# Kernel optimization log

Measured on AMD Instinct MI355X. Metric: run time of the kernel, lower is better.

## Reference

```python
import jax, jax.numpy as jnp
import numpy as np

GRID_SIZE = 3
SPLINE_ORDER = 3

def make_grid():
    # grid_range=[-1,1], h=2/grid_size; extended grid of length grid_size+2k+1 = 10
    h = 2.0 / GRID_SIZE
    return (jnp.arange(-SPLINE_ORDER, GRID_SIZE + SPLINE_ORDER + 1, dtype=jnp.float32) * h - 1.0)

def b_splines(x, grid):
    # x: [N, F] -> bases [N, F, grid_size+spline_order]
    xg = x[..., None]
    bases = ((xg >= grid[:-1]) & (xg < grid[1:])).astype(x.dtype)
    for j in range(1, SPLINE_ORDER + 1):
        left = (xg - grid[: -(j + 1)]) / (grid[j:-1] - grid[: -(j + 1)])
        right = (grid[j + 1:] - xg) / (grid[j + 1:] - grid[1:-j])
        bases = left * bases[..., :-1] + right * bases[..., 1:]
    return bases

def kan_linear(x, base_w, spline_w, scaler, grid):
    # x: [N, F]; base_w: [O, F]; spline_w: [O, F, G]; scaler: [O, F]
    base = jax.nn.silu(x) @ base_w.T
    sb = b_splines(x, grid)                      # [N, F, G]
    spl = jnp.einsum('nfg,ofg->no', sb, spline_w * scaler[..., None])
    return base + spl

def kan_conv3x3(x, base_w, spline_w, scaler, grid):
    # x: [B, C, H, W]; 3x3 kernel, pad 1, stride 1 -> [B, O, H, W]
    B, C, H, W = x.shape
    patches = jax.lax.conv_general_dilated_patches(
        x, (3, 3), (1, 1), ((1, 1), (1, 1)))     # [B, C*9, H, W]
    p = patches.transpose(0, 2, 3, 1).reshape(B * H * W, C * 9)
    y = kan_linear(p, base_w, spline_w, scaler, grid)
    return y.reshape(B, H, W, -1).transpose(0, 3, 1, 2)

def maxpool2(x):
    return jax.lax.reduce_window(x, -jnp.inf, jax.lax.max,
                                 (1, 1, 2, 2), (1, 1, 2, 2), 'VALID')

def setup_inputs() -> dict:
    key = jax.random.key(0)
    ks = jax.random.split(key, 12)
    s = 0.1
    return {
        'x': jax.random.normal(ks[0], (256, 3, 32, 32), jnp.float32),
        'c1_base_w': jax.random.normal(ks[1], (8, 27), jnp.float32) * s,
        'c1_spline_w': jax.random.normal(ks[2], (8, 27, 6), jnp.float32) * s,
        'c1_scaler': jax.random.normal(ks[3], (8, 27), jnp.float32) * s,
        'c2_base_w': jax.random.normal(ks[4], (16, 72), jnp.float32) * s,
        'c2_spline_w': jax.random.normal(ks[5], (16, 72, 6), jnp.float32) * s,
        'c2_scaler': jax.random.normal(ks[6], (16, 72), jnp.float32) * s,
        'c3_base_w': jax.random.normal(ks[7], (32, 144), jnp.float32) * s,
        'c3_spline_w': jax.random.normal(ks[8], (32, 144, 6), jnp.float32) * s,
        'c3_scaler': jax.random.normal(ks[9], (32, 144), jnp.float32) * s,
        'lin_w': jax.random.normal(ks[10], (100, 512), jnp.float32) * s,
        'lin_b': jax.random.normal(ks[11], (100,), jnp.float32) * s,
    }

def reference(x, c1_base_w, c1_spline_w, c1_scaler,
              c2_base_w, c2_spline_w, c2_scaler,
              c3_base_w, c3_spline_w, c3_scaler,
              lin_w, lin_b):
    grid = make_grid()
    h = maxpool2(kan_conv3x3(x, c1_base_w, c1_spline_w, c1_scaler, grid))   # [B,8,16,16]
    h = maxpool2(kan_conv3x3(h, c2_base_w, c2_spline_w, c2_scaler, grid))   # [B,16,8,8]
    h = maxpool2(kan_conv3x3(h, c3_base_w, c3_spline_w, c3_scaler, grid))   # [B,32,4,4]
    h = h.reshape(h.shape[0], -1)                                           # [B,512]
    return h @ lin_w.T + lin_b                                              # [B,100]
```

## Files before the change

### kernel.cpp

```cpp
#include <hip/hip_runtime.h>
#include <math.h>


#define BATCH 256

typedef short bf16x8 __attribute__((ext_vector_type(8)));
typedef float f32x4  __attribute__((ext_vector_type(4)));

__device__ __forceinline__ unsigned f2bf(float f) {
    unsigned u = __float_as_uint(f);
    u += 0x7fffu + ((u >> 16) & 1u);
    return u >> 16;
}
__device__ __forceinline__ unsigned pk2(float a, float b) {
    return f2bf(a) | (f2bf(b) << 16);
}

__device__ __forceinline__ void bspline_basis(float x, float bs[6]) {
    const float h = 2.0f / 3.0f;
    float g[10];
#pragma unroll
    for (int i = 0; i < 10; ++i) g[i] = (float)(i - 3) * h - 1.0f;
    float b[9];
#pragma unroll
    for (int i = 0; i < 9; ++i) b[i] = (x >= g[i] && x < g[i + 1]) ? 1.0f : 0.0f;
#pragma unroll
    for (int j = 1; j <= 3; ++j) {
        const float inv_d = 1.0f / ((float)j * h);
#pragma unroll
        for (int i = 0; i + j < 9; ++i) {
            float left  = (x - g[i]) * inv_d;
            float right = (g[i + j + 1] - x) * inv_d;
            b[i] = left * b[i] + right * b[i + 1];
        }
    }
#pragma unroll
    for (int i = 0; i < 6; ++i) bs[i] = b[i];
}

__device__ __forceinline__ uint4 act_record(float val) {
    float silu = val / (1.0f + __expf(-val));
    float bs[6];
    bspline_basis(val, bs);
    uint4 r;
    r.x = pk2(silu, bs[0]);
    r.y = pk2(bs[1], bs[2]);
    r.z = pk2(bs[3], bs[4]);
    r.w = f2bf(bs[5]);
    return r;
}

__device__ __forceinline__ uint4 fuse_w(const float* bw, const float* sw,
                                        const float* sc, int j) {
    float s = sc[j];
    uint4 r;
    r.x = pk2(bw[j],             sw[j * 6 + 0] * s);
    r.y = pk2(sw[j * 6 + 1] * s, sw[j * 6 + 2] * s);
    r.z = pk2(sw[j * 6 + 3] * s, sw[j * 6 + 4] * s);
    r.w = f2bf(sw[j * 6 + 5] * s);
    return r;
}

__global__ __launch_bounds__(512, 4) void kan_l1(
        const float* __restrict__ x,
        const float* __restrict__ bw, const float* __restrict__ sw,
        const float* __restrict__ sc,
        const float* __restrict__ bw3, const float* __restrict__ sw3,
        const float* __restrict__ sc3,
        uint4* __restrict__ w3g,
        float* __restrict__ out) {
    constexpr int C = 3, H = 32, W = 32, F = 27, FP = 28, NS = 7;
    constexpr int RT = 18, TC = 34, NT = 512;

    __shared__ uint4 s_act[C * RT * TC];
    __shared__ uint4 s_w[FP * 16];

    const int tid = threadIdx.x;
    const int bid = blockIdx.x;
    const int b   = bid >> 1;
    const int v   = bid & 1;

    if (bid < 9) {
        int i = bid * NT + tid;
        if (i < 4608) {
            int o = i / 144, fp = i % 144;
            w3g[fp * 32 + o] = fuse_w(bw3, sw3, sc3, i);
        }
    }

    for (int i = tid; i < FP * 16; i += NT) {
        int fp = i >> 4, o = i & 15;
        uint4 r = make_uint4(0u, 0u, 0u, 0u);
        if (fp < F && o < 8) r = fuse_w(bw, sw, sc, o * F + fp);
        s_w[i] = r;
    }

    const int r0 = 16 * v - 1;
    const float* xb = x + (size_t)b * C * H * W;
    for (int i = tid; i < C * RT * TC; i += NT) {
        int cc  = i / (RT * TC);
        int rr  = (i / TC) % RT;
        int col = i % TC;
        int gr = r0 + rr, gc = col - 1;
        float val = 0.0f;
        if ((unsigned)gr < (unsigned)H && (unsigned)gc < (unsigned)W)
            val = xb[(cc * H + gr) * W + gc];
        s_act[i] = act_record(val);
    }
    __syncthreads();

    const int lane = tid & 63;
    const int wv   = tid >> 6;
    const int kg   = lane >> 4;
    const int oc   = lane & 15;
    const int m    = lane & 15;

    bf16x8 bfr[NS];
#pragma unroll
    for (int s = 0; s < NS; ++s)
        bfr[s] = *reinterpret_cast<const bf16x8*>(&s_w[(4 * s + kg) * 16 + oc]);

    int pixoff[4];
#pragma unroll
    for (int t = 0; t < 4; ++t)
        pixoff[t] = (2 * wv + (t >> 1)) * TC + 16 * (t & 1) + m;

    f32x4 acc[4];
#pragma unroll
    for (int t = 0; t < 4; ++t) acc[t] = (f32x4){0.f, 0.f, 0.f, 0.f};

#pragma unroll
    for (int s = 0; s < NS; ++s) {
        int tp = 4 * s + kg;
        tp = (tp > F - 1) ? F - 1 : tp;
        int c  = tp / 9;
        int t9 = tp - 9 * c;
        int ky = t9 / 3;
        int kx = t9 - 3 * ky;
        int base = (c * RT + ky) * TC + kx;
#pragma unroll
        for (int t = 0; t < 4; ++t) {
            bf16x8 a = *reinterpret_cast<const bf16x8*>(&s_act[base + pixoff[t]]);
            acc[t] = __builtin_amdgcn_mfma_f32_16x16x32_bf16(a, bfr[s], acc[t], 0, 0, 0);
        }
    }

    if (oc < 8) {
        f32x4 e0, e1;
#pragma unroll
        for (int p = 0; p < 4; ++p) {
            e0[p] = fmaxf(acc[0][p], acc[2][p]);
            e1[p] = fmaxf(acc[1][p], acc[3][p]);
        }
        float* op = out + (((size_t)b * 8 + oc) * 16 + (8 * v + wv)) * 16;
        op[2 * kg]         = fmaxf(e0[0], e0[1]);
        op[2 * kg + 1]     = fmaxf(e0[2], e0[3]);
        op[8 + 2 * kg]     = fmaxf(e1[0], e1[1]);
        op[8 + 2 * kg + 1] = fmaxf(e1[2], e1[3]);
    }
}

__global__ __launch_bounds__(512, 2) void kan_l2l3lin(
        const float* __restrict__ h1,
        const float* __restrict__ bw2, const float* __restrict__ sw2,
        const float* __restrict__ sc2,
        const uint4* __restrict__ w3g,
        const float* __restrict__ lin_w, const float* __restrict__ lin_b,
        float* __restrict__ out) {
    constexpr int NT = 512;
    __shared__ alignas(16) unsigned char s_mem[59904];
    uint4* s_act2 = (uint4*)s_mem;
    uint4* s_w2   = (uint4*)(s_mem + 41472);
    float* s_h2   = (float*)s_mem;
    uint4* s_act3 = (uint4*)(s_mem + 4096);
    float* s_h3   = (float*)s_mem;

    const int tid = threadIdx.x;
    const int n   = blockIdx.x;
    const int lane = tid & 63;
    const int wv   = tid >> 6;
    const int kg   = lane >> 4;
    const int oc   = lane & 15;
    const int m    = lane & 15;

    for (int i = tid; i < 72 * 16; i += NT) {
        int fp = i >> 4, o = i & 15;
        s_w2[i] = fuse_w(bw2, sw2, sc2, o * 72 + fp);
    }
    const float* xb = h1 + (size_t)n * 8 * 16 * 16;
    for (int i = tid; i < 8 * 18 * 18; i += NT) {
        int cc  = i / 324;
        int rr  = (i / 18) % 18;
        int col = i % 18;
        int gr = rr - 1, gc = col - 1;
        float val = 0.0f;
        if ((unsigned)gr < 16u && (unsigned)gc < 16u)
            val = xb[(cc * 16 + gr) * 16 + gc];
        s_act2[i] = act_record(val);
    }
    __syncthreads();

    {
        bf16x8 bfr2[18];
#pragma unroll
        for (int s = 0; s < 18; ++s)
            bfr2[s] = *reinterpret_cast<const bf16x8*>(&s_w2[(4 * s + kg) * 16 + oc]);
        const int p0 = (2 * wv) * 18 + m;
        const int p1 = p0 + 18;
        f32x4 a0 = (f32x4){0.f, 0.f, 0.f, 0.f}, a1 = a0, b0 = a0, b1 = a0;
#pragma unroll
        for (int s = 0; s < 18; ++s) {
            int tp = 4 * s + kg;
            int c  = tp / 9;
            int t9 = tp - 9 * c;
            int ky = t9 / 3;
            int kx = t9 - 3 * ky;
            int base = (c * 18 + ky) * 18 + kx;
            bf16x8 av0 = *reinterpret_cast<const bf16x8*>(&s_act2[base + p0]);
            bf16x8 av1 = *reinterpret_cast<const bf16x8*>(&s_act2[base + p1]);
            if (s < 9) {
                a0 = __builtin_amdgcn_mfma_f32_16x16x32_bf16(av0, bfr2[s], a0, 0, 0, 0);
                a1 = __builtin_amdgcn_mfma_f32_16x16x32_bf16(av1, bfr2[s], a1, 0, 0, 0);
            } else {
                b0 = __builtin_amdgcn_mfma_f32_16x16x32_bf16(av0, bfr2[s], b0, 0, 0, 0);
                b1 = __builtin_amdgcn_mfma_f32_16x16x32_bf16(av1, bfr2[s], b1, 0, 0, 0);
            }
        }
        a0 = a0 + b0;
        a1 = a1 + b1;
        float e0 = fmaxf(a0[0], a1[0]);
        float e1 = fmaxf(a0[1], a1[1]);
        float e2 = fmaxf(a0[2], a1[2]);
        float e3 = fmaxf(a0[3], a1[3]);
        __syncthreads();
        s_h2[(oc * 8 + wv) * 8 + 2 * kg]     = fmaxf(e0, e1);
        s_h2[(oc * 8 + wv) * 8 + 2 * kg + 1] = fmaxf(e2, e3);
    }
    __syncthreads();

    for (int i = tid; i < 16 * 10 * 10; i += NT) {
        int cc  = i / 100;
        int rr  = (i / 10) % 10;
        int col = i % 10;
        int gr = rr - 1, gc = col - 1;
        float val = 0.0f;
        if ((unsigned)gr < 8u && (unsigned)gc < 8u)
            val = s_h2[(cc * 8 + gr) * 8 + gc];
        s_act3[i] = act_record(val);
    }
    __syncthreads();

    {
        const int mt  = wv & 3;
        const int o03 = 16 * (wv >> 2);
        bf16x8 bfr3[36];
#pragma unroll
        for (int s = 0; s < 36; ++s)
            bfr3[s] = *reinterpret_cast<const bf16x8*>(&w3g[(4 * s + kg) * 32 + o03 + oc]);
        const int poff = (2 * mt + (m >> 3)) * 10 + (m & 7);
        f32x4 a3 = (f32x4){0.f, 0.f, 0.f, 0.f}, a3b = a3;
#pragma unroll
        for (int s = 0; s < 36; ++s) {
            int tp = 4 * s + kg;
            int c  = tp / 9;
            int t9 = tp - 9 * c;
            int ky = t9 / 3;
            int kx = t9 - 3 * ky;
            int base = (c * 10 + ky) * 10 + kx;
            bf16x8 av = *reinterpret_cast<const bf16x8*>(&s_act3[base + poff]);
            if (s < 18)
                a3 = __builtin_amdgcn_mfma_f32_16x16x32_bf16(av, bfr3[s], a3, 0, 0, 0);
            else
                a3b = __builtin_amdgcn_mfma_f32_16x16x32_bf16(av, bfr3[s], a3b, 0, 0, 0);
        }
        a3 = a3 + a3b;
        float q0 = fmaxf(a3[0], a3[1]);
        float q1 = fmaxf(a3[2], a3[3]);
        float y0 = fmaxf(q0, __shfl_xor(q0, 32));
        float y1 = fmaxf(q1, __shfl_xor(q1, 32));
        if (kg < 2) {
            s_h3[(o03 + oc) * 16 + mt * 4 + 2 * kg]     = y0;
            s_h3[(o03 + oc) * 16 + mt * 4 + 2 * kg + 1] = y1;
        }
    }
    __syncthreads();

    {
        const float4* hf = (const float4*)s_h3;
        const float4 h0v = hf[lane];
        const float4 h1v = hf[lane + 64];
        const float4* wr = (const float4*)(lin_w + (size_t)wv * 512);
        float4 w0 = wr[lane];
        float4 w1 = wr[lane + 64];
#pragma unroll 1
        for (int o = wv; o < 100; o += 8) {
            float4 nw0, nw1;
            const int on = o + 8;
            if (on < 100) {
                const float4* wn = (const float4*)(lin_w + (size_t)on * 512);
                nw0 = wn[lane];
                nw1 = wn[lane + 64];
            }
            float p = w0.x * h0v.x + w0.y * h0v.y + w0.z * h0v.z + w0.w * h0v.w
                    + w1.x * h1v.x + w1.y * h1v.y + w1.z * h1v.z + w1.w * h1v.w;
            p += __shfl_xor(p, 32);
            p += __shfl_xor(p, 16);
            p += __shfl_xor(p, 8);
            p += __shfl_xor(p, 4);
            p += __shfl_xor(p, 2);
            p += __shfl_xor(p, 1);
            if (lane == 0) out[(size_t)n * 100 + o] = p + lin_b[o];
            w0 = nw0;
            w1 = nw1;
        }
    }
}

extern "C" void kernel_launch(void* const* d_in, const int* in_sizes, int n_in,
                              void* d_out, int out_size, void* d_ws, size_t ws_size,
                              hipStream_t stream) {
    const float* x     = (const float*)d_in[0];
    const float* c1_bw = (const float*)d_in[1];
    const float* c1_sw = (const float*)d_in[2];
    const float* c1_sc = (const float*)d_in[3];
    const float* c2_bw = (const float*)d_in[4];
    const float* c2_sw = (const float*)d_in[5];
    const float* c2_sc = (const float*)d_in[6];
    const float* c3_bw = (const float*)d_in[7];
    const float* c3_sw = (const float*)d_in[8];
    const float* c3_sc = (const float*)d_in[9];
    const float* lin_w = (const float*)d_in[10];
    const float* lin_b = (const float*)d_in[11];
    float* out = (float*)d_out;

    float* ws = (float*)d_ws;
    float* h1 = ws;
    uint4* w3g = (uint4*)(h1 + 524288);

    kan_l1<<<512, 512, 0, stream>>>(x, c1_bw, c1_sw, c1_sc,
                                    c3_bw, c3_sw, c3_sc, w3g, h1);
    kan_l2l3lin<<<256, 512, 0, stream>>>(h1, c2_bw, c2_sw, c2_sc,
                                         w3g, lin_w, lin_b, out);
}
```

Baseline: 105.7 us.

## Split second kernel into two half-image blocks per sample with atomic linear output

The fused layer-2/3/linear kernel now runs two blocks per image, each handling half the rows with halo recomputation. Layer 3 splits the K dimension across wave groups and reduces the partials through shared memory, and the final linear layer accumulates each half's contribution with atomicAdd into an output that the first kernel zeroes. Shared memory drops and the launch bound rises so more blocks fit per CU, aiming for better occupancy across 256 CUs. In exchange, three of eight waves sit idle in layer 2, halo rows are recomputed, and atomics make the output accumulation order nondeterministic.

```diff
diff --git a/kernel.cpp b/kernel.cpp
--- a/kernel.cpp
+++ b/kernel.cpp
@@ -68,6 +68,7 @@
         const float* __restrict__ bw3, const float* __restrict__ sw3,
         const float* __restrict__ sc3,
         uint4* __restrict__ w3g,
+        float* __restrict__ lin_out,
         float* __restrict__ out) {
     constexpr int C = 3, H = 32, W = 32, F = 27, FP = 28, NS = 7;
     constexpr int RT = 18, TC = 34, NT = 512;
@@ -86,6 +87,10 @@
             int o = i / 144, fp = i % 144;
             w3g[fp * 32 + o] = fuse_w(bw3, sw3, sc3, i);
         }
+    }
+    if (bid >= 16 && bid < 66) {
+        int i = (bid - 16) * NT + tid;
+        if (i < BATCH * 100) lin_out[i] = 0.0f;
     }
 
     for (int i = tid; i < FP * 16; i += NT) {
@@ -160,7 +165,7 @@
     }
 }
 
-__global__ __launch_bounds__(512, 2) void kan_l2l3lin(
+__global__ __launch_bounds__(512, 4) void kan_l2l3lin(
         const float* __restrict__ h1,
         const float* __restrict__ bw2, const float* __restrict__ sw2,
         const float* __restrict__ sc2,
@@ -168,15 +173,18 @@
         const float* __restrict__ lin_w, const float* __restrict__ lin_b,
         float* __restrict__ out) {
     constexpr int NT = 512;
-    __shared__ alignas(16) unsigned char s_mem[59904];
+    __shared__ alignas(16) unsigned char s_mem[46080];
     uint4* s_act2 = (uint4*)s_mem;
-    uint4* s_w2   = (uint4*)(s_mem + 41472);
+    uint4* s_w2   = (uint4*)(s_mem + 27648);
     float* s_h2   = (float*)s_mem;
     uint4* s_act3 = (uint4*)(s_mem + 4096);
+    f32x4* s_part = (f32x4*)(s_mem + 19456);
     float* s_h3   = (float*)s_mem;
 
     const int tid = threadIdx.x;
-    const int n   = blockIdx.x;
+    const int bid = blockIdx.x;
+    const int n   = bid >> 1;
+    const int hh  = bid & 1;
     const int lane = tid & 63;
     const int wv   = tid >> 6;
     const int kg   = lane >> 4;
@@ -188,11 +196,11 @@
         s_w2[i] = fuse_w(bw2, sw2, sc2, o * 72 + fp);
     }
     const float* xb = h1 + (size_t)n * 8 * 16 * 16;
-    for (int i = tid; i < 8 * 18 * 18; i += NT) {
-        int cc  = i / 324;
-        int rr  = (i / 18) % 18;
+    for (int i = tid; i < 1728; i += NT) {
+        int cc  = i / 216;
+        int rr  = (i / 18) % 12;
         int col = i % 18;
-        int gr = rr - 1, gc = col - 1;
+        int gr = 6 * hh - 1 + rr, gc = col - 1;
         float val = 0.0f;
         if ((unsigned)gr < 16u && (unsigned)gc < 16u)
             val = xb[(cc * 16 + gr) * 16 + gc];
@@ -200,7 +208,8 @@
     }
     __syncthreads();
 
-    {
+    float e0 = 0.f, e1 = 0.f, e2 = 0.f, e3 = 0.f;
+    if (wv < 5) {
         bf16x8 bfr2[18];
 #pragma unroll
         for (int s = 0; s < 18; ++s)
@@ -215,7 +224,7 @@
             int t9 = tp - 9 * c;
             int ky = t9 / 3;
             int kx = t9 - 3 * ky;
-            int base = (c * 18 + ky) * 18 + kx;
+            int base = c * 216 + ky * 18 + kx;
             bf16x8 av0 = *reinterpret_cast<const bf16x8*>(&s_act2[base + p0]);
             bf16x8 av1 = *reinterpret_cast<const bf16x8*>(&s_act2[base + p1]);
             if (s < 9) {
@@ -228,90 +237,92 @@
         }
         a0 = a0 + b0;
         a1 = a1 + b1;
-        float e0 = fmaxf(a0[0], a1[0]);
-        float e1 = fmaxf(a0[1], a1[1]);
-        float e2 = fmaxf(a0[2], a1[2]);
-        float e3 = fmaxf(a0[3], a1[3]);
-        __syncthreads();
-        s_h2[(oc * 8 + wv) * 8 + 2 * kg]     = fmaxf(e0, e1);
-        s_h2[(oc * 8 + wv) * 8 + 2 * kg + 1] = fmaxf(e2, e3);
-    }
-    __syncthreads();
-
-    for (int i = tid; i < 16 * 10 * 10; i += NT) {
-        int cc  = i / 100;
-        int rr  = (i / 10) % 10;
+        e0 = fmaxf(a0[0], a1[0]);
+        e1 = fmaxf(a0[1], a1[1]);
+        e2 = fmaxf(a0[2], a1[2]);
+        e3 = fmaxf(a0[3], a1[3]);
+    }
+    __syncthreads();
+    if (wv < 5) {
+        const int prow = 3 * hh + wv;
+        s_h2[(oc * 8 + prow) * 8 + 2 * kg]     = fmaxf(e0, e1);
+        s_h2[(oc * 8 + prow) * 8 + 2 * kg + 1] = fmaxf(e2, e3);
+    }
+    __syncthreads();
+
+    for (int i = tid; i < 960; i += NT) {
+        int cc  = i / 60;
+        int lr  = (i / 10) % 6;
         int col = i % 10;
-        int gr = rr - 1, gc = col - 1;
+        int hr = 4 * hh - 1 + lr, gc = col - 1;
         float val = 0.0f;
-        if ((unsigned)gr < 8u && (unsigned)gc < 8u)
-            val = s_h2[(cc * 8 + gr) * 8 + gc];
+        if ((unsigned)hr < 8u && (unsigned)gc < 8u)
+            val = s_h2[(cc * 8 + hr) * 8 + gc];
         s_act3[i] = act_record(val);
     }
     __syncthreads();
 
     {
-        const int mt  = wv & 3;
-        const int o03 = 16 * (wv >> 2);
-        bf16x8 bfr3[36];
-#pragma unroll
-        for (int s = 0; s < 36; ++s)
-            bfr3[s] = *reinterpret_cast<const bf16x8*>(&w3g[(4 * s + kg) * 32 + o03 + oc]);
-        const int poff = (2 * mt + (m >> 3)) * 10 + (m & 7);
+        const int mt_l = wv & 1;
+        const int o03  = 16 * ((wv >> 1) & 1);
+        const int kh   = wv >> 2;
+        bf16x8 bfr3[18];
+#pragma unroll
+        for (int s = 0; s < 18; ++s)
+            bfr3[s] = *reinterpret_cast<const bf16x8*>(
+                &w3g[(4 * (s + 18 * kh) + kg) * 32 + o03 + oc]);
+        const int poff = (2 * mt_l + (m >> 3)) * 10 + (m & 7);
         f32x4 a3 = (f32x4){0.f, 0.f, 0.f, 0.f}, a3b = a3;
 #pragma unroll
-        for (int s = 0; s < 36; ++s) {
-            int tp = 4 * s + kg;
+        for (int s = 0; s < 18; ++s) {
+            int tp = 4 * (s + 18 * kh) + kg;
             int c  = tp / 9;
             int t9 = tp - 9 * c;
             int ky = t9 / 3;
             int kx = t9 - 3 * ky;
-            int base = (c * 10 + ky) * 10 + kx;
+            int base = (c * 6 + ky) * 10 + kx;
             bf16x8 av = *reinterpret_cast<const bf16x8*>(&s_act3[base + poff]);
-            if (s < 18)
+            if (s < 9)
                 a3 = __builtin_amdgcn_mfma_f32_16x16x32_bf16(av, bfr3[s], a3, 0, 0, 0);
             else
                 a3b = __builtin_amdgcn_mfma_f32_16x16x32_bf16(av, bfr3[s], a3b, 0, 0, 0);
         }
         a3 = a3 + a3b;
-        float q0 = fmaxf(a3[0], a3[1]);
-        float q1 = fmaxf(a3[2], a3[3]);
-        float y0 = fmaxf(q0, __shfl_xor(q0, 32));
-        float y1 = fmaxf(q1, __shfl_xor(q1, 32));
-        if (kg < 2) {
-            s_h3[(o03 + oc) * 16 + mt * 4 + 2 * kg]     = y0;
-            s_h3[(o03 + oc) * 16 + mt * 4 + 2 * kg + 1] = y1;
+        if (kh == 1) s_part[(wv - 4) * 64 + lane] = a3;
+        __syncthreads();
+        if (kh == 0) {
+            f32x4 t = s_part[wv * 64 + lane];
+            a3 = a3 + t;
+            float q0 = fmaxf(a3[0], a3[1]);
+            float q1 = fmaxf(a3[2], a3[3]);
+            float y0 = fmaxf(q0, __shfl_xor(q0, 32));
+            float y1 = fmaxf(q1, __shfl_xor(q1, 32));
+            const int mtg = 2 * hh + mt_l;
+            if (kg < 2) {
+                s_h3[(o03 + oc) * 16 + mtg * 4 + 2 * kg]     = y0;
+                s_h3[(o03 + oc) * 16 + mtg * 4 + 2 * kg + 1] = y1;
+            }
         }
     }
     __syncthreads();
 
     {
         const float4* hf = (const float4*)s_h3;
-        const float4 h0v = hf[lane];
-        const float4 h1v = hf[lane + 64];
-        const float4* wr = (const float4*)(lin_w + (size_t)wv * 512);
-        float4 w0 = wr[lane];
-        float4 w1 = wr[lane + 64];
+        const int fidx = (lane >> 1) * 4 + 2 * hh + (lane & 1);
+        const float4 hv = hf[fidx];
 #pragma unroll 1
         for (int o = wv; o < 100; o += 8) {
-            float4 nw0, nw1;
-            const int on = o + 8;
-            if (on < 100) {
-                const float4* wn = (const float4*)(lin_w + (size_t)on * 512);
-                nw0 = wn[lane];
-                nw1 = wn[lane + 64];
-            }
-            float p = w0.x * h0v.x + w0.y * h0v.y + w0.z * h0v.z + w0.w * h0v.w
-                    + w1.x * h1v.x + w1.y * h1v.y + w1.z * h1v.z + w1.w * h1v.w;
+            const float4 w0 = ((const float4*)(lin_w + (size_t)o * 512))[fidx];
+            float p = w0.x * hv.x + w0.y * hv.y + w0.z * hv.z + w0.w * hv.w;
             p += __shfl_xor(p, 32);
             p += __shfl_xor(p, 16);
             p += __shfl_xor(p, 8);
             p += __shfl_xor(p, 4);
             p += __shfl_xor(p, 2);
             p += __shfl_xor(p, 1);
-            if (lane == 0) out[(size_t)n * 100 + o] = p + lin_b[o];
-            w0 = nw0;
-            w1 = nw1;
+            if (lane == 0)
+                atomicAdd(&out[(size_t)n * 100 + o],
+                          p + (hh == 0 ? lin_b[o] : 0.0f));
         }
     }
 }
@@ -338,7 +349,7 @@
     uint4* w3g = (uint4*)(h1 + 524288);
 
     kan_l1<<<512, 512, 0, stream>>>(x, c1_bw, c1_sw, c1_sc,
-                                    c3_bw, c3_sw, c3_sc, w3g, h1);
-    kan_l2l3lin<<<256, 512, 0, stream>>>(h1, c2_bw, c2_sw, c2_sc,
+                                    c3_bw, c3_sw, c3_sc, w3g, out, h1);
+    kan_l2l3lin<<<512, 512, 0, stream>>>(h1, c2_bw, c2_sw, c2_sc,
                                          w3g, lin_w, lin_b, out);
 }
```

Measured after the change: 109.9 us. 4.0% more time.
